# Kernel tuning notes

Measured on AMD Instinct MI355X. Metric: run time of the kernel, lower is better.

## Reference

```python
import jax, jax.numpy as jnp
import numpy as np

N_NODES, N_EDGES, CH, FEAT = 20000, 320000, 256, 118


def setup_inputs() -> dict:
    key = jax.random.key(0)
    ks = jax.random.split(key, 8)
    x = jax.random.uniform(ks[0], (N_NODES, FEAT), dtype=jnp.float32)
    edge_index = jax.random.randint(ks[1], (2, N_EDGES), 0, N_NODES, dtype=jnp.int64)
    s = 0.05
    W_embed = jax.random.normal(ks[2], (FEAT, CH), dtype=jnp.float32) * s
    b_embed = jnp.zeros((CH,), jnp.float32)
    W1 = jax.random.normal(ks[3], (CH, CH), dtype=jnp.float32) * s
    b1 = jnp.zeros((CH,), jnp.float32)
    W2 = jax.random.normal(ks[4], (CH, CH), dtype=jnp.float32) * s
    b2 = jnp.zeros((CH,), jnp.float32)
    return {"x": x, "edge_index": edge_index, "W_embed": W_embed, "b_embed": b_embed,
            "W1": W1, "b1": b1, "W2": W2, "b2": b2}


def reference(x, edge_index, W_embed, b_embed, W1, b1, W2, b2):
    n = x.shape[0]
    # node embedding: Linear(118 -> C)
    h = x @ W_embed + b_embed  # [N, C]
    src, dst = edge_index[0], edge_index[1]
    # message: gather x_j per edge, dense1 + exact GELU (dropout = identity in eval)
    msg = jax.nn.gelu(h[src] @ W1 + b1, approximate=False)  # [E, C]
    # mean aggregation into destination nodes
    agg = jax.ops.segment_sum(msg, dst, num_segments=n)  # [N, C]
    cnt = jax.ops.segment_sum(jnp.ones((msg.shape[0],), msg.dtype), dst, num_segments=n)
    agg = agg / jnp.maximum(cnt, 1.0)[:, None]
    # update: dense2 + exact GELU
    out = jax.nn.gelu(agg @ W2 + b2, approximate=False)  # [N, C]
    # final mean over channel dim
    return out.mean(axis=1)  # [N]
```

## Files before the change

### kernel.cpp

```cpp
#include <hip/hip_runtime.h>
#include <math.h>

#define N_NODES 20000
#define N_EDGES 320000
#define CH      256
#define FEAT    118
#define CAP     48

typedef float    f32x4 __attribute__((ext_vector_type(4)));
typedef short    s16x8 __attribute__((ext_vector_type(8)));
typedef _Float16 f16x4 __attribute__((ext_vector_type(4)));
typedef unsigned short u16;

union Frag { s16x8 v; u16 u[8]; };

__device__ __forceinline__ float gelu_exact(float x) {
    return 0.5f * x * (1.0f + erff(x * 0.70710678118654752f));
}
__device__ __forceinline__ u16 f2bf(float f) {
    unsigned u = __float_as_uint(f);
    u = (u + 0x7FFFu + ((u >> 16) & 1u)) >> 16;
    return (u16)u;
}
__device__ __forceinline__ float bf2f(u16 h) { return __uint_as_float(((unsigned)h) << 16); }

__global__ __launch_bounds__(256) void prep(const float* __restrict__ x,
                                            const int* __restrict__ ei,
                                            const float* __restrict__ We,
                                            const float* __restrict__ be,
                                            const float* __restrict__ W1,
                                            const float* __restrict__ b1,
                                            const float* __restrict__ W2,
                                            u16* __restrict__ xh, u16* __restrict__ xl,
                                            int* __restrict__ cnt, int* __restrict__ bins,
                                            u16* __restrict__ w2h, u16* __restrict__ w2l,
                                            u16* __restrict__ wch, u16* __restrict__ wcl,
                                            float* __restrict__ bc) {
    const int b = blockIdx.x, tid = threadIdx.x;
    if (b < 1250) {
        int fid = b * 256 + tid;
        int lane = fid & 63, ks = (fid >> 6) & 3, mt = fid >> 8;
        int row = mt * 16 + (lane & 15);
        int k0 = ks * 32 + (lane >> 4) * 8;
        Frag hi, lo;
        #pragma unroll
        for (int j = 0; j < 8; j++) {
            int k = k0 + j;
            float v = (k < FEAT) ? x[(size_t)row * FEAT + k] : 0.0f;
            u16 h = f2bf(v);
            hi.u[j] = h; lo.u[j] = f2bf(v - bf2f(h));
        }
        ((s16x8*)xh)[fid] = hi.v;
        ((s16x8*)xl)[fid] = lo.v;
    } else if (b < 2500) {
        int e = (b - 1250) * 256 + tid;
        int s = ei[e];
        int d = ei[N_EDGES + e];
        int p = atomicAdd(&cnt[d], 1);
        if (p < CAP) bins[(size_t)d * CAP + p] = s;
    } else if (b < 2532) {
        int fid = (b - 2500) * 256 + tid;
        int lane = fid & 63, ks = (fid >> 6) & 7, nt = fid >> 9;
        int n = nt * 16 + (lane & 15);
        int k0 = ks * 32 + (lane >> 4) * 8;
        Frag hi, lo;
        #pragma unroll
        for (int j = 0; j < 8; j++) {
            float v = W2[(size_t)(k0 + j) * 256 + n];
            u16 h = f2bf(v);
            hi.u[j] = h; lo.u[j] = f2bf(v - bf2f(h));
        }
        ((s16x8*)w2h)[fid] = hi.v;
        ((s16x8*)w2l)[fid] = lo.v;
    } else {
        int f = b - 2532;
        int n = tid;
        if (f < 128) {
            float acc = 0.0f;
            if (f < FEAT) {
                const float* wr = We + (size_t)f * 256;
                #pragma unroll 8
                for (int c = 0; c < 256; c++) acc += wr[c] * W1[(size_t)c * 256 + n];
            }
            int nt = n >> 4, lm = n & 15, ks = f >> 5, q = (f >> 3) & 3, j = f & 7;
            size_t idx = (((size_t)nt * 4 + ks) * 64 + q * 16 + lm) * 8 + j;
            u16 h = f2bf(acc);
            wch[idx] = h;
            wcl[idx] = f2bf(acc - bf2f(h));
        } else {
            float acc = b1[n];
            #pragma unroll 8
            for (int c = 0; c < 256; c++) acc += be[c] * W1[(size_t)c * 256 + n];
            bc[n] = acc;
        }
    }
}

__global__ __launch_bounds__(256) void gemm_main(const u16* __restrict__ Ah_, const u16* __restrict__ Al_,
                                                 const u16* __restrict__ Bh_, const u16* __restrict__ Bl_,
                                                 const float* __restrict__ bias,
                                                 _Float16* __restrict__ Mout) {
    __shared__ _Float16 Ls[32][256];
    const int tid = threadIdx.x, wave = tid >> 6, lane = tid & 63;
    const int quad = lane >> 4, lm = lane & 15;
    const int mt0 = blockIdx.x * 2, nt0 = wave * 4;
    const s16x8* Ah = (const s16x8*)Ah_; const s16x8* Al = (const s16x8*)Al_;
    const s16x8* Bh = (const s16x8*)Bh_; const s16x8* Bl = (const s16x8*)Bl_;
    f32x4 acc[2][4];
    #pragma unroll
    for (int mi = 0; mi < 2; mi++)
        #pragma unroll
        for (int t = 0; t < 4; t++) acc[mi][t] = f32x4{0.f, 0.f, 0.f, 0.f};
    #pragma unroll
    for (int ks = 0; ks < 4; ks++) {
        s16x8 a0h = Ah[((size_t)(mt0 + 0) * 4 + ks) * 64 + lane];
        s16x8 a0l = Al[((size_t)(mt0 + 0) * 4 + ks) * 64 + lane];
        s16x8 a1h = Ah[((size_t)(mt0 + 1) * 4 + ks) * 64 + lane];
        s16x8 a1l = Al[((size_t)(mt0 + 1) * 4 + ks) * 64 + lane];
        #pragma unroll
        for (int t = 0; t < 4; t++) {
            s16x8 bh = Bh[((size_t)(nt0 + t) * 4 + ks) * 64 + lane];
            s16x8 bl = Bl[((size_t)(nt0 + t) * 4 + ks) * 64 + lane];
            acc[0][t] = __builtin_amdgcn_mfma_f32_16x16x32_bf16(a0h, bh, acc[0][t], 0, 0, 0);
            acc[0][t] = __builtin_amdgcn_mfma_f32_16x16x32_bf16(a0l, bh, acc[0][t], 0, 0, 0);
            acc[0][t] = __builtin_amdgcn_mfma_f32_16x16x32_bf16(a0h, bl, acc[0][t], 0, 0, 0);
            acc[1][t] = __builtin_amdgcn_mfma_f32_16x16x32_bf16(a1h, bh, acc[1][t], 0, 0, 0);
            acc[1][t] = __builtin_amdgcn_mfma_f32_16x16x32_bf16(a1l, bh, acc[1][t], 0, 0, 0);
            acc[1][t] = __builtin_amdgcn_mfma_f32_16x16x32_bf16(a1h, bl, acc[1][t], 0, 0, 0);
        }
    }
    #pragma unroll
    for (int t = 0; t < 4; t++) {
        float bn = bias[(nt0 + t) * 16 + lm];
        #pragma unroll
        for (int mi = 0; mi < 2; mi++)
            #pragma unroll
            for (int r = 0; r < 4; r++)
                Ls[mi * 16 + quad * 4 + r][(nt0 + t) * 16 + lm] =
                    (_Float16)gelu_exact(acc[mi][t][r] + bn);
    }
    __syncthreads();
    s16x8* dst = (s16x8*)Mout + (size_t)blockIdx.x * 1024;
    const s16x8* src = (const s16x8*)&Ls[0][0];
    #pragma unroll
    for (int it = 0; it < 4; it++)
        dst[it * 256 + tid] = src[it * 256 + tid];
}

__global__ __launch_bounds__(256) void aggregate(const _Float16* __restrict__ M,
                                                 const int* __restrict__ cnt,
                                                 const int* __restrict__ bins,
                                                 u16* __restrict__ Ah, u16* __restrict__ Al) {
    int node = (blockIdx.x * 256 + threadIdx.x) >> 6;
    int lane = threadIdx.x & 63;
    int c = cnt[node];
    int cc = min(c, CAP);
    int myid = (lane < CAP) ? bins[(size_t)node * CAP + lane] : 0;
    float acc[4][4];
    #pragma unroll
    for (int u = 0; u < 4; u++)
        #pragma unroll
        for (int q = 0; q < 4; q++) acc[u][q] = 0.0f;
    int j = 0;
    for (; j + 4 <= cc; j += 4) {
        #pragma unroll
        for (int u = 0; u < 4; u++) {
            int s = __shfl(myid, j + u, 64);
            f16x4 v = *(const f16x4*)(M + (size_t)s * CH + lane * 4);
            acc[u][0] += (float)v.x; acc[u][1] += (float)v.y;
            acc[u][2] += (float)v.z; acc[u][3] += (float)v.w;
        }
    }
    for (; j < cc; j++) {
        int s = __shfl(myid, j, 64);
        f16x4 v = *(const f16x4*)(M + (size_t)s * CH + lane * 4);
        acc[0][0] += (float)v.x; acc[0][1] += (float)v.y;
        acc[0][2] += (float)v.z; acc[0][3] += (float)v.w;
    }
    float inv = 1.0f / (float)max(c, 1);
    float vv[4];
    #pragma unroll
    for (int q = 0; q < 4; q++)
        vv[q] = (acc[0][q] + acc[1][q] + acc[2][q] + acc[3][q]) * inv;
    int mt = node >> 4, lm = node & 15;
    int ks = lane >> 3, quad = (lane & 7) >> 1, j0 = (lane & 1) * 4;
    size_t base = (((size_t)mt * 8 + ks) * 64 + quad * 16 + lm) * 8 + j0;
    ushort4 hv, lv;
    u16* hp = (u16*)&hv; u16* lp = (u16*)&lv;
    #pragma unroll
    for (int q = 0; q < 4; q++) {
        u16 h = f2bf(vv[q]);
        hp[q] = h; lp[q] = f2bf(vv[q] - bf2f(h));
    }
    *(ushort4*)(Ah + base) = hv;
    *(ushort4*)(Al + base) = lv;
}

__global__ __launch_bounds__(256) void gemm_mean(const u16* __restrict__ Ah_, const u16* __restrict__ Al_,
                                                 const u16* __restrict__ Bh_, const u16* __restrict__ Bl_,
                                                 const float* __restrict__ bias,
                                                 float* __restrict__ out) {
    __shared__ float part[4][32];
    const int tid = threadIdx.x, wave = tid >> 6, lane = tid & 63;
    const int quad = lane >> 4, lm = lane & 15;
    const int mt0 = blockIdx.x * 2, nt0 = wave * 4;
    const s16x8* Ah = (const s16x8*)Ah_; const s16x8* Al = (const s16x8*)Al_;
    const s16x8* Bh = (const s16x8*)Bh_; const s16x8* Bl = (const s16x8*)Bl_;
    f32x4 acc[2][4];
    #pragma unroll
    for (int mi = 0; mi < 2; mi++)
        #pragma unroll
        for (int t = 0; t < 4; t++) acc[mi][t] = f32x4{0.f, 0.f, 0.f, 0.f};
    #pragma unroll
    for (int ks = 0; ks < 8; ks++) {
        s16x8 a0h = Ah[((size_t)(mt0 + 0) * 8 + ks) * 64 + lane];
        s16x8 a0l = Al[((size_t)(mt0 + 0) * 8 + ks) * 64 + lane];
        s16x8 a1h = Ah[((size_t)(mt0 + 1) * 8 + ks) * 64 + lane];
        s16x8 a1l = Al[((size_t)(mt0 + 1) * 8 + ks) * 64 + lane];
        #pragma unroll
        for (int t = 0; t < 4; t++) {
            s16x8 bh = Bh[((size_t)(nt0 + t) * 8 + ks) * 64 + lane];
            s16x8 bl = Bl[((size_t)(nt0 + t) * 8 + ks) * 64 + lane];
            acc[0][t] = __builtin_amdgcn_mfma_f32_16x16x32_bf16(a0h, bh, acc[0][t], 0, 0, 0);
            acc[0][t] = __builtin_amdgcn_mfma_f32_16x16x32_bf16(a0l, bh, acc[0][t], 0, 0, 0);
            acc[0][t] = __builtin_amdgcn_mfma_f32_16x16x32_bf16(a0h, bl, acc[0][t], 0, 0, 0);
            acc[1][t] = __builtin_amdgcn_mfma_f32_16x16x32_bf16(a1h, bh, acc[1][t], 0, 0, 0);
            acc[1][t] = __builtin_amdgcn_mfma_f32_16x16x32_bf16(a1l, bh, acc[1][t], 0, 0, 0);
            acc[1][t] = __builtin_amdgcn_mfma_f32_16x16x32_bf16(a1h, bl, acc[1][t], 0, 0, 0);
        }
    }
    float p[2][4] = {{0.f,0.f,0.f,0.f},{0.f,0.f,0.f,0.f}};
    #pragma unroll
    for (int t = 0; t < 4; t++) {
        float bn = bias[(nt0 + t) * 16 + lm];
        #pragma unroll
        for (int mi = 0; mi < 2; mi++)
            #pragma unroll
            for (int r = 0; r < 4; r++)
                p[mi][r] += gelu_exact(acc[mi][t][r] + bn);
    }
    #pragma unroll
    for (int off = 1; off < 16; off <<= 1)
        #pragma unroll
        for (int mi = 0; mi < 2; mi++)
            #pragma unroll
            for (int r = 0; r < 4; r++)
                p[mi][r] += __shfl_xor(p[mi][r], off, 64);
    if (lm == 0)
        #pragma unroll
        for (int mi = 0; mi < 2; mi++)
            #pragma unroll
            for (int r = 0; r < 4; r++)
                part[wave][mi * 16 + quad * 4 + r] = p[mi][r];
    __syncthreads();
    if (tid < 32) {
        float s = part[0][tid] + part[1][tid] + part[2][tid] + part[3][tid];
        out[blockIdx.x * 32 + tid] = s * (1.0f / 256.0f);
    }
}

extern "C" void kernel_launch(void* const* d_in, const int* in_sizes, int n_in,
                              void* d_out, int out_size, void* d_ws, size_t ws_size,
                              hipStream_t stream) {
    const float* x  = (const float*)d_in[0];
    const int*   ei = (const int*)d_in[1];
    const float* We = (const float*)d_in[2];
    const float* be = (const float*)d_in[3];
    const float* W1 = (const float*)d_in[4];
    const float* b1 = (const float*)d_in[5];
    const float* W2 = (const float*)d_in[6];
    const float* b2 = (const float*)d_in[7];
    float* out = (float*)d_out;

    char* ws = (char*)d_ws;
    size_t off = 0;
    u16* xh = (u16*)(ws + off);
    u16* aggh = (u16*)(ws + off); off += 5120000;
    u16* xl = (u16*)(ws + off); off += 5120000;
    _Float16* M = (_Float16*)(ws + off); off += 10240000;
    u16* aggl = (u16*)(ws + off); off += 10240000;
    u16* wch = (u16*)(ws + off); off += 65536;
    u16* wcl = (u16*)(ws + off); off += 65536;
    u16* w2h = (u16*)(ws + off); off += 131072;
    u16* w2l = (u16*)(ws + off); off += 131072;
    float* bc = (float*)(ws + off); off += 1024;
    int* cnt  = (int*)(ws + off); off += N_NODES * 4;
    int* bins = (int*)(ws + off); off += (size_t)N_NODES * CAP * 4;

    hipMemsetAsync(cnt, 0, N_NODES * sizeof(int), stream);
    prep<<<2661, 256, 0, stream>>>(x, ei, We, be, W1, b1, W2,
                                   xh, xl, cnt, bins, w2h, w2l, wch, wcl, bc);
    gemm_main<<<N_NODES / 32, 256, 0, stream>>>(xh, xl, wch, wcl, bc, M);
    aggregate<<<N_NODES / 4, 256, 0, stream>>>(M, cnt, bins, aggh, aggl);
    gemm_mean<<<N_NODES / 32, 256, 0, stream>>>(aggh, aggl, w2h, w2l, b2, out);
}
```

Baseline: 155.5 us.

## Store aggregated features as fp16 and split to bf16 hi/lo inside gemm_mean

The aggregate kernel now writes a single row-major fp16 mean per node instead of two bf16 hi/lo arrays in MFMA fragment layout. gemm_mean stages each 32-row tile in LDS and does the bf16 hi/lo split in registers before the MFMAs. The gather loop is also restructured to issue 8 loads per batch before accumulating. This is meant to cut the intermediate write and read traffic, at the cost of fp16 rounding of the aggregate, extra conversion ALU work and LDS staging in the GEMM.

```diff
diff --git a/kernel.cpp b/kernel.cpp
--- a/kernel.cpp
+++ b/kernel.cpp
@@ -10,6 +10,7 @@
 typedef float    f32x4 __attribute__((ext_vector_type(4)));
 typedef short    s16x8 __attribute__((ext_vector_type(8)));
 typedef _Float16 f16x4 __attribute__((ext_vector_type(4)));
+typedef _Float16 f16x8 __attribute__((ext_vector_type(8)));
 typedef unsigned short u16;
 
 union Frag { s16x8 v; u16 u[8]; };
@@ -23,6 +24,17 @@
     return (u16)u;
 }
 __device__ __forceinline__ float bf2f(u16 h) { return __uint_as_float(((unsigned)h) << 16); }
+
+__device__ __forceinline__ void cvt_split(f16x8 a, s16x8& hi, s16x8& lo) {
+    Frag H, L;
+    #pragma unroll
+    for (int e = 0; e < 8; e++) {
+        float v = (float)a[e];
+        u16 h = f2bf(v);
+        H.u[e] = h; L.u[e] = f2bf(v - bf2f(h));
+    }
+    hi = H.v; lo = L.v;
+}
 
 __global__ __launch_bounds__(256) void prep(const float* __restrict__ x,
                                             const int* __restrict__ ei,
@@ -150,61 +162,55 @@
 __global__ __launch_bounds__(256) void aggregate(const _Float16* __restrict__ M,
                                                  const int* __restrict__ cnt,
                                                  const int* __restrict__ bins,
-                                                 u16* __restrict__ Ah, u16* __restrict__ Al) {
+                                                 _Float16* __restrict__ agg) {
     int node = (blockIdx.x * 256 + threadIdx.x) >> 6;
     int lane = threadIdx.x & 63;
     int c = cnt[node];
     int cc = min(c, CAP);
     int myid = (lane < CAP) ? bins[(size_t)node * CAP + lane] : 0;
-    float acc[4][4];
-    #pragma unroll
-    for (int u = 0; u < 4; u++)
-        #pragma unroll
-        for (int q = 0; q < 4; q++) acc[u][q] = 0.0f;
-    int j = 0;
-    for (; j + 4 <= cc; j += 4) {
-        #pragma unroll
-        for (int u = 0; u < 4; u++) {
-            int s = __shfl(myid, j + u, 64);
-            f16x4 v = *(const f16x4*)(M + (size_t)s * CH + lane * 4);
-            acc[u][0] += (float)v.x; acc[u][1] += (float)v.y;
-            acc[u][2] += (float)v.z; acc[u][3] += (float)v.w;
-        }
-    }
-    for (; j < cc; j++) {
-        int s = __shfl(myid, j, 64);
-        f16x4 v = *(const f16x4*)(M + (size_t)s * CH + lane * 4);
-        acc[0][0] += (float)v.x; acc[0][1] += (float)v.y;
-        acc[0][2] += (float)v.z; acc[0][3] += (float)v.w;
+    float a0 = 0.f, a1 = 0.f, a2 = 0.f, a3 = 0.f;
+    for (int j = 0; j < cc; j += 8) {
+        f16x4 v[8];
+        #pragma unroll
+        for (int u = 0; u < 8; u++) {
+            int s = __shfl(myid, min(j + u, cc - 1), 64);
+            v[u] = *(const f16x4*)(M + (size_t)s * CH + lane * 4);
+        }
+        #pragma unroll
+        for (int u = 0; u < 8; u++) {
+            if (j + u < cc) {
+                a0 += (float)v[u].x; a1 += (float)v[u].y;
+                a2 += (float)v[u].z; a3 += (float)v[u].w;
+            }
+        }
     }
     float inv = 1.0f / (float)max(c, 1);
-    float vv[4];
-    #pragma unroll
-    for (int q = 0; q < 4; q++)
-        vv[q] = (acc[0][q] + acc[1][q] + acc[2][q] + acc[3][q]) * inv;
-    int mt = node >> 4, lm = node & 15;
-    int ks = lane >> 3, quad = (lane & 7) >> 1, j0 = (lane & 1) * 4;
-    size_t base = (((size_t)mt * 8 + ks) * 64 + quad * 16 + lm) * 8 + j0;
-    ushort4 hv, lv;
-    u16* hp = (u16*)&hv; u16* lp = (u16*)&lv;
-    #pragma unroll
-    for (int q = 0; q < 4; q++) {
-        u16 h = f2bf(vv[q]);
-        hp[q] = h; lp[q] = f2bf(vv[q] - bf2f(h));
-    }
-    *(ushort4*)(Ah + base) = hv;
-    *(ushort4*)(Al + base) = lv;
-}
-
-__global__ __launch_bounds__(256) void gemm_mean(const u16* __restrict__ Ah_, const u16* __restrict__ Al_,
+    f16x4 o;
+    o.x = (_Float16)(a0 * inv); o.y = (_Float16)(a1 * inv);
+    o.z = (_Float16)(a2 * inv); o.w = (_Float16)(a3 * inv);
+    *(f16x4*)(agg + (size_t)node * CH + lane * 4) = o;
+}
+
+#define LPITCH 264
+__global__ __launch_bounds__(256) void gemm_mean(const _Float16* __restrict__ agg,
                                                  const u16* __restrict__ Bh_, const u16* __restrict__ Bl_,
                                                  const float* __restrict__ bias,
                                                  float* __restrict__ out) {
+    __shared__ _Float16 Ls[32][LPITCH];
     __shared__ float part[4][32];
     const int tid = threadIdx.x, wave = tid >> 6, lane = tid & 63;
     const int quad = lane >> 4, lm = lane & 15;
-    const int mt0 = blockIdx.x * 2, nt0 = wave * 4;
-    const s16x8* Ah = (const s16x8*)Ah_; const s16x8* Al = (const s16x8*)Al_;
+    const int nt0 = wave * 4;
+    {
+        const f16x8* src = (const f16x8*)(agg + (size_t)blockIdx.x * 32 * CH);
+        #pragma unroll
+        for (int it = 0; it < 4; it++) {
+            int id = it * 256 + tid;
+            int row = id >> 5, seg = id & 31;
+            *(f16x8*)&Ls[row][seg * 8] = src[id];
+        }
+    }
+    __syncthreads();
     const s16x8* Bh = (const s16x8*)Bh_; const s16x8* Bl = (const s16x8*)Bl_;
     f32x4 acc[2][4];
     #pragma unroll
@@ -213,10 +219,10 @@
         for (int t = 0; t < 4; t++) acc[mi][t] = f32x4{0.f, 0.f, 0.f, 0.f};
     #pragma unroll
     for (int ks = 0; ks < 8; ks++) {
-        s16x8 a0h = Ah[((size_t)(mt0 + 0) * 8 + ks) * 64 + lane];
-        s16x8 a0l = Al[((size_t)(mt0 + 0) * 8 + ks) * 64 + lane];
-        s16x8 a1h = Ah[((size_t)(mt0 + 1) * 8 + ks) * 64 + lane];
-        s16x8 a1l = Al[((size_t)(mt0 + 1) * 8 + ks) * 64 + lane];
+        int c0 = ks * 32 + quad * 8;
+        s16x8 a0h, a0l, a1h, a1l;
+        cvt_split(*(const f16x8*)&Ls[lm][c0],      a0h, a0l);
+        cvt_split(*(const f16x8*)&Ls[16 + lm][c0], a1h, a1l);
         #pragma unroll
         for (int t = 0; t < 4; t++) {
             s16x8 bh = Bh[((size_t)(nt0 + t) * 8 + ks) * 64 + lane];
@@ -275,10 +281,10 @@
     char* ws = (char*)d_ws;
     size_t off = 0;
     u16* xh = (u16*)(ws + off);
-    u16* aggh = (u16*)(ws + off); off += 5120000;
+    _Float16* agg = (_Float16*)(ws + off);
+    off += 5120000;
     u16* xl = (u16*)(ws + off); off += 5120000;
     _Float16* M = (_Float16*)(ws + off); off += 10240000;
-    u16* aggl = (u16*)(ws + off); off += 10240000;
     u16* wch = (u16*)(ws + off); off += 65536;
     u16* wcl = (u16*)(ws + off); off += 65536;
     u16* w2h = (u16*)(ws + off); off += 131072;
@@ -291,6 +297,6 @@
     prep<<<2661, 256, 0, stream>>>(x, ei, We, be, W1, b1, W2,
                                    xh, xl, cnt, bins, w2h, w2l, wch, wcl, bc);
     gemm_main<<<N_NODES / 32, 256, 0, stream>>>(xh, xl, wch, wcl, bc, M);
-    aggregate<<<N_NODES / 4, 256, 0, stream>>>(M, cnt, bins, aggh, aggl);
-    gemm_mean<<<N_NODES / 32, 256, 0, stream>>>(aggh, aggl, w2h, w2l, b2, out);
-}
+    aggregate<<<N_NODES / 4, 256, 0, stream>>>(M, cnt, bins, agg);
+    gemm_mean<<<N_NODES / 32, 256, 0, stream>>>(agg, w2h, w2l, b2, out);
+}
```

After: 158.6 us. No clear change (+2.0%).
